# Performance work log

Hardware: AMD Instinct MI355X
Metric: run time of the kernel (lower is better)

## Reference

```python
import jax, jax.numpy as jnp
import numpy as np

# NLMConv1DBlock: NLM LogicMachine(depth=2, breadth=2, input_dims=[0, inp_dim, 3],
# output_dims=[D,D,D], logic_hidden_dim=None -> each logic MLP is Linear+Sigmoid),
# followed by swish -> Conv1d(D, D, k=3, pad=1) over the t axis -> swish.
# Only the unary (arity-1) output of the second NLM layer is consumed, so the
# nullary/binary heads of layer 2 are never computed (their params are unused).


def swish(x):
    return x * jax.nn.sigmoid(x)


def lin_sig(x, W, b):
    # LogicInference with logic_hidden_dim=None: single Linear + Sigmoid
    return jax.nn.sigmoid(x @ W.T + b)


def reduce_unary(f1):
    # Reducer(dim=1): [B, n, C] -> [B, 2C]; exclude_self is a no-op for arity 1.
    # Channels interleaved as (exists_0, forall_0, exists_1, forall_1, ...)
    e = jnp.max(f1, axis=1)
    a = jnp.min(f1, axis=1)
    return jnp.stack([e, a], axis=-1).reshape(f1.shape[0], -1)


def reduce_pair(f2):
    # Reducer(dim=2, exclude_self=True): [B, n, n, C] -> [B, n, 2C].
    # Diagonal (i==j) masked to 0 for exists(max) and 1 for forall(min);
    # reduction over the second object index (axis=2). Interleaved exists/forall.
    n = f2.shape[1]
    eye = jnp.eye(n, dtype=bool)[None, :, :, None]
    e = jnp.max(jnp.where(eye, jnp.zeros((), f2.dtype), f2), axis=2)
    a = jnp.min(jnp.where(eye, jnp.ones((), f2.dtype), f2), axis=2)
    return jnp.stack([e, a], axis=-1).reshape(f2.shape[0], n, -1)


def perm2(f2):
    # Permutation(dim=2): concat identity and object-dim transpose along channels
    return jnp.concatenate([f2, jnp.swapaxes(f2, 1, 2)], axis=-1)


def setup_inputs() -> dict:
    key = jax.random.key(0)
    ks = jax.random.split(key, 12)
    b, t, n, inp_dim, D = 16, 16, 64, 2, 32
    s = 0.1
    x = jax.random.normal(ks[0], (b, t, n, inp_dim), jnp.float32)
    # Layer 1 logic MLPs (forward concat order: [expand, input, reduce])
    W1_0 = jax.random.normal(ks[1], (D, 2 * inp_dim), jnp.float32) * s        # nullary: reduce(unary) -> 2*inp_dim
    b1_0 = jax.random.normal(ks[2], (D,), jnp.float32) * s
    W1_1 = jax.random.normal(ks[3], (D, inp_dim + 6), jnp.float32) * s        # unary: [x, reduce(cmp)] -> inp_dim + 2*3
    b1_1 = jax.random.normal(ks[4], (D,), jnp.float32) * s
    W1_2 = jax.random.normal(ks[5], (D, 2 * (inp_dim + 3)), jnp.float32) * s  # binary: perm2([expand(x), cmp])
    b1_2 = jax.random.normal(ks[6], (D,), jnp.float32) * s
    # Layer 2, only the unary head is used downstream
    W2_1 = jax.random.normal(ks[7], (D, 4 * D), jnp.float32) * s              # [expand(g0), g1, reduce(g2)]
    b2_1 = jax.random.normal(ks[8], (D,), jnp.float32) * s
    # Conv1d(D, D, kernel_size=3, padding=1), OIH layout
    Wc = jax.random.normal(ks[9], (D, D, 3), jnp.float32) * s
    bc = jax.random.normal(ks[10], (D,), jnp.float32) * s
    return {"x": x, "W1_0": W1_0, "b1_0": b1_0, "W1_1": W1_1, "b1_1": b1_1,
            "W1_2": W1_2, "b1_2": b1_2, "W2_1": W2_1, "b2_1": b2_1,
            "Wc": Wc, "bc": bc}


def reference(x, W1_0, b1_0, W1_1, b1_1, W1_2, b1_2, W2_1, b2_1, Wc, bc):
    b, t, n, c = x.shape
    B = b * t
    xf = x.reshape(B, n, c)

    # pairwise relational inputs: [B, n, n, 3]
    ar = jnp.arange(n)
    base = jnp.stack([ar[:, None] < ar[None, :], ar[:, None] == ar[None, :]],
                     axis=-1).astype(x.dtype)                       # [n, n, 2], batch-invariant
    numbers = xf[:, :, 1]
    cmp3 = (numbers[:, :, None] < numbers[:, None, :]).astype(x.dtype)
    cmp = jnp.concatenate([jnp.broadcast_to(base[None], (B, n, n, 2)),
                           cmp3[..., None]], axis=-1)

    # --- NLM layer 1 (input dims [0, c, 3]) ---
    g0 = lin_sig(reduce_unary(xf), W1_0, b1_0)                                # [B, D]
    g1 = lin_sig(jnp.concatenate([xf, reduce_pair(cmp)], axis=-1), W1_1, b1_1)  # [B, n, D]
    f2 = jnp.concatenate([jnp.broadcast_to(xf[:, :, None, :], (B, n, n, c)), cmp], axis=-1)
    g2 = lin_sig(perm2(f2), W1_2, b1_2)                                       # [B, n, n, D]

    # --- NLM layer 2, unary head only (block takes nlm(...)[1]) ---
    D = g1.shape[-1]
    h1_in = jnp.concatenate([jnp.broadcast_to(g0[:, None, :], (B, n, D)),
                             g1, reduce_pair(g2)], axis=-1)                   # [B, n, 4D]
    h1 = swish(lin_sig(h1_in, W2_1, b2_1))                                    # [B, n, D]

    # (b t) n c -> (b n) c t, conv1d over t, -> b t n c, swish
    y = h1.reshape(b, t, n, D).transpose(0, 2, 3, 1).reshape(b * n, D, t)
    y = jax.lax.conv_general_dilated(y, Wc, (1,), [(1, 1)],
                                     dimension_numbers=('NCH', 'OIH', 'NCH'))
    y = y + bc[None, :, None]
    y = y.reshape(b, n, D, t).transpose(0, 3, 1, 2)
    return swish(y)
```

## Files before the change

### kernel.cpp

```cpp
#include <hip/hip_runtime.h>

#define NN 64
#define DD 32

__device__ __forceinline__ float sigmoidf_(float x) {
    return 1.0f / (1.0f + __expf(-x));
}

__device__ __forceinline__ float rlanef_(float v, int l) {
    return __int_as_float(__builtin_amdgcn_readlane(__float_as_int(v), l));
}

__global__ __launch_bounds__(1024) void stage1_kernel(
    const float* __restrict__ x,
    const float* __restrict__ W1_0, const float* __restrict__ b1_0,
    const float* __restrict__ W1_1, const float* __restrict__ b1_1,
    const float* __restrict__ W1_2, const float* __restrict__ b1_2,
    const float* __restrict__ W2_1, const float* __restrict__ b2_1,
    float* __restrict__ h1ws)
{
    __shared__ __align__(16) float sx0[NN];
    __shared__ __align__(16) float sx1[NN];
    __shared__ __align__(16) float sFeat[NN][100];
    __shared__ __align__(16) float sW2p[DD][100];
    __shared__ float sW12[DD*10];
    __shared__ float sB12[DD];
    __shared__ float sW11t[8*DD];
    __shared__ float sB11[DD];
    __shared__ float sG0[DD];
    __shared__ float sZ0[DD];
    __shared__ float sEC2[NN];
    __shared__ float sAC2[NN];

    const int tid = threadIdx.x;
    const int bb  = blockIdx.x;
    const int d   = tid & 31;

    if (tid < NN) {
        sx0[tid] = x[(bb*NN + tid)*2 + 0];
        sx1[tid] = x[(bb*NN + tid)*2 + 1];
    }
    for (int idx = tid; idx < DD*96; idx += 1024) {
        int dr = idx / 96, kp = idx - dr*96;
        sW2p[dr][kp] = W2_1[dr*128 + 32 + kp];
    }
    if (tid < 320) {
        sW12[tid] = W1_2[tid];
    } else if (tid < 352) {
        sB12[tid - 320] = b1_2[tid - 320];
    } else if (tid < 608) {
        int idx = tid - 352; int dr = idx >> 3, c = idx & 7;
        sW11t[c*DD + dr] = W1_1[idx];
    } else if (tid < 640) {
        sB11[tid - 608] = b1_1[tid - 608];
    }
    __syncthreads();

    const float myx0 = sx0[tid & 63];
    const float myx1 = sx1[tid & 63];

    const float w0 = sW12[d*10+0], w1 = sW12[d*10+1], w2 = sW12[d*10+2],
                w4 = sW12[d*10+4], w5 = sW12[d*10+5], w6 = sW12[d*10+6],
                w7 = sW12[d*10+7], w9 = sW12[d*10+9];
    const float bw = sB12[d];

    if (tid < NN) {
        float ni = sx1[tid];
        float mx = -1e30f, mn = 1e30f;
        for (int j = 0; j < NN; ++j) {
            float nj = sx1[j];
            bool v = (j != tid);
            mx = fmaxf(mx, v ? nj : -1e30f);
            mn = fminf(mn, v ? nj :  1e30f);
        }
        sEC2[tid] = (ni < mx) ? 1.0f : 0.0f;
        sAC2[tid] = (ni < mn) ? 1.0f : 0.0f;
    } else if (tid < 96) {
        int dd = tid - 64;
        float mx0 = -1e30f, mn0 = 1e30f, mx1 = -1e30f, mn1 = 1e30f;
        for (int j = 0; j < NN; ++j) {
            float a = sx0[j], c = sx1[j];
            mx0 = fmaxf(mx0, a); mn0 = fminf(mn0, a);
            mx1 = fmaxf(mx1, c); mn1 = fminf(mn1, c);
        }
        float z = mx0*W1_0[dd*4+0] + mn0*W1_0[dd*4+1]
                + mx1*W1_0[dd*4+2] + mn1*W1_0[dd*4+3] + b1_0[dd];
        sG0[dd] = sigmoidf_(z);
    }
    __syncthreads();

    if (tid < 32) {
        float z = b2_1[tid];
        const float* wr = W2_1 + tid*128;
        #pragma unroll
        for (int k = 0; k < 32; ++k) z += sG0[k]*wr[k];
        sZ0[tid] = z;
    }

    {
        const int ia = tid >> 5;
        const int ib = ia + 32;
        const float na = sx1[ia], nb = sx1[ib];
        const float Aa = sx0[ia]*w0 + na*w1 + bw;
        const float Ab = sx0[ib]*w0 + nb*w1 + bw;
        const float A24a = Aa + w2 + w4, A29a = Aa + w2 + w9;
        const float A74a = Aa + w7 + w4, A79a = Aa + w7 + w9;
        const float A24b = Ab + w2 + w4, A29b = Ab + w2 + w9;
        const float A74b = Ab + w7 + w4, A79b = Ab + w7 + w9;
        float smaxa = -1e30f, smina = 1e30f;
        float smaxb = -1e30f, sminb = 1e30f;

        #pragma unroll
        for (int j = 0; j < 32; ++j) {
            const float x0j = rlanef_(myx0, j);
            const float x1j = rlanef_(myx1, j);
            const float bv  = x0j*w5 + x1j*w6;
            const float tb = ((nb < x1j) ? A74b : A79b) + bv;
            smaxb = fmaxf(smaxb, tb);
            sminb = fminf(sminb, tb);
            const bool ca = (na < x1j);
            const float t2 = ca ? A24a : A29a;
            const float t7 = ca ? A74a : A79a;
            const float ta = ((ia < j) ? t2 : t7) + bv;
            const bool va = (j != ia);
            smaxa = fmaxf(smaxa, va ? ta : -1e30f);
            smina = fminf(smina, va ? ta :  1e30f);
        }
        #pragma unroll
        for (int j = 32; j < 64; ++j) {
            const float x0j = rlanef_(myx0, j);
            const float x1j = rlanef_(myx1, j);
            const float bv  = x0j*w5 + x1j*w6;
            const float ta = ((na < x1j) ? A24a : A29a) + bv;
            smaxa = fmaxf(smaxa, ta);
            smina = fminf(smina, ta);
            const bool cb = (nb < x1j);
            const float t2 = cb ? A24b : A29b;
            const float t7 = cb ? A74b : A79b;
            const float tb = ((ib < j) ? t2 : t7) + bv;
            const bool vb = (j != ib);
            smaxb = fmaxf(smaxb, vb ? tb : -1e30f);
            sminb = fminf(sminb, vb ? tb :  1e30f);
        }
        *(float2*)&sFeat[ia][32 + 2*d] = make_float2(sigmoidf_(smaxa), sigmoidf_(smina));
        *(float2*)&sFeat[ib][32 + 2*d] = make_float2(sigmoidf_(smaxb), sigmoidf_(sminb));

        float z1a = sx0[ia]*sW11t[0*DD+d] + na*sW11t[1*DD+d]
                  + sW11t[2*DD+d]
                  + ((ia == 0) ? sW11t[3*DD+d] : 0.0f)
                  + sEC2[ia]*sW11t[6*DD+d] + sAC2[ia]*sW11t[7*DD+d] + sB11[d];
        sFeat[ia][d] = sigmoidf_(z1a);
        float z1b = sx0[ib]*sW11t[0*DD+d] + nb*sW11t[1*DD+d]
                  + ((ib < NN-1) ? sW11t[2*DD+d] : 0.0f)
                  + sEC2[ib]*sW11t[6*DD+d] + sAC2[ib]*sW11t[7*DD+d] + sB11[d];
        sFeat[ib][d] = sigmoidf_(z1b);
    }
    __syncthreads();

    if (tid < 256) {
        const int i0 = tid >> 4;
        const int dh = tid & 15;
        const float* f0 = sFeat[i0];
        const float* f1 = sFeat[i0+16];
        const float* f2 = sFeat[i0+32];
        const float* f3 = sFeat[i0+48];
        const float* wA = sW2p[dh];
        const float* wB = sW2p[dh+16];
        const float z0A = sZ0[dh], z0B = sZ0[dh+16];
        float a0A = z0A, a0B = z0B, a1A = z0A, a1B = z0B;
        float a2A = z0A, a2B = z0B, a3A = z0A, a3B = z0B;
        #pragma unroll
        for (int kc = 0; kc < 96; kc += 4) {
            const float4 pa = *(const float4*)(wA + kc);
            const float4 pb = *(const float4*)(wB + kc);
            const float4 v0 = *(const float4*)(f0 + kc);
            const float4 v1 = *(const float4*)(f1 + kc);
            const float4 v2 = *(const float4*)(f2 + kc);
            const float4 v3 = *(const float4*)(f3 + kc);
            a0A += v0.x*pa.x + v0.y*pa.y + v0.z*pa.z + v0.w*pa.w;
            a0B += v0.x*pb.x + v0.y*pb.y + v0.z*pb.z + v0.w*pb.w;
            a1A += v1.x*pa.x + v1.y*pa.y + v1.z*pa.z + v1.w*pa.w;
            a1B += v1.x*pb.x + v1.y*pb.y + v1.z*pb.z + v1.w*pb.w;
            a2A += v2.x*pa.x + v2.y*pa.y + v2.z*pa.z + v2.w*pa.w;
            a2B += v2.x*pb.x + v2.y*pb.y + v2.z*pb.z + v2.w*pb.w;
            a3A += v3.x*pa.x + v3.y*pa.y + v3.z*pa.z + v3.w*pa.w;
            a3B += v3.x*pb.x + v3.y*pb.y + v3.z*pb.z + v3.w*pb.w;
        }
        float* orow = h1ws + bb*(NN*DD);
        float h;
        h = sigmoidf_(a0A); orow[ i0     *DD + dh]      = h * sigmoidf_(h);
        h = sigmoidf_(a0B); orow[ i0     *DD + dh + 16] = h * sigmoidf_(h);
        h = sigmoidf_(a1A); orow[(i0+16)*DD + dh]       = h * sigmoidf_(h);
        h = sigmoidf_(a1B); orow[(i0+16)*DD + dh + 16]  = h * sigmoidf_(h);
        h = sigmoidf_(a2A); orow[(i0+32)*DD + dh]       = h * sigmoidf_(h);
        h = sigmoidf_(a2B); orow[(i0+32)*DD + dh + 16]  = h * sigmoidf_(h);
        h = sigmoidf_(a3A); orow[(i0+48)*DD + dh]       = h * sigmoidf_(h);
        h = sigmoidf_(a3B); orow[(i0+48)*DD + dh + 16]  = h * sigmoidf_(h);
    }
}

__global__ __launch_bounds__(512) void conv_kernel(
    const float* __restrict__ h1ws,
    const float* __restrict__ Wc,
    const float* __restrict__ bc,
    float* __restrict__ out)
{
    __shared__ __align__(16) float sh[4][18][32];

    const int tid = threadIdx.x;
    const int blk = blockIdx.x;
    const int b   = blk >> 4;
    const int n0  = (blk & 15) * 4;
    const int t   = tid >> 5;
    const int dd  = tid & 31;

    float wreg[96];
    {
        const float* wrow = Wc + dd*96;
        #pragma unroll
        for (int c = 0; c < 24; ++c) {
            float4 v = *(const float4*)(wrow + c*4);
            wreg[c*4+0] = v.x; wreg[c*4+1] = v.y;
            wreg[c*4+2] = v.z; wreg[c*4+3] = v.w;
        }
    }
    for (int idx = tid; idx < 4*16*32; idx += 512) {
        int nl = idx >> 9; int rem = idx & 511;
        int tl = rem >> 5; int dl = rem & 31;
        sh[nl][tl+1][dl] = h1ws[((b*16 + tl)*NN + (n0+nl))*DD + dl];
    }
    if (tid < 256) {
        int nl = tid >> 6; int r = tid & 63;
        int row = (r >> 5) * 17; int dl = r & 31;
        sh[nl][row][dl] = 0.0f;
    }
    const float bcv = bc[dd];
    __syncthreads();

    #pragma unroll
    for (int g = 0; g < 4; ++g) {
        float acc = bcv;
        const float* r0 = &sh[g][t][0];
        const float* r1 = &sh[g][t+1][0];
        const float* r2 = &sh[g][t+2][0];
        #pragma unroll
        for (int c = 0; c < 8; ++c) {
            float4 f0  = *(const float4*)(r0 + c*4);
            float4 f1  = *(const float4*)(r1 + c*4);
            float4 f2v = *(const float4*)(r2 + c*4);
            const int q = c*12;
            acc += f0.x*wreg[q+0] + f1.x*wreg[q+1]  + f2v.x*wreg[q+2];
            acc += f0.y*wreg[q+3] + f1.y*wreg[q+4]  + f2v.y*wreg[q+5];
            acc += f0.z*wreg[q+6] + f1.z*wreg[q+7]  + f2v.z*wreg[q+8];
            acc += f0.w*wreg[q+9] + f1.w*wreg[q+10] + f2v.w*wreg[q+11];
        }
        out[((b*16 + t)*NN + (n0+g))*DD + dd] = acc * sigmoidf_(acc);
    }
}

extern "C" void kernel_launch(void* const* d_in, const int* in_sizes, int n_in,
                              void* d_out, int out_size, void* d_ws, size_t ws_size,
                              hipStream_t stream) {
    const float* x    = (const float*)d_in[0];
    const float* W1_0 = (const float*)d_in[1];
    const float* b1_0 = (const float*)d_in[2];
    const float* W1_1 = (const float*)d_in[3];
    const float* b1_1 = (const float*)d_in[4];
    const float* W1_2 = (const float*)d_in[5];
    const float* b1_2 = (const float*)d_in[6];
    const float* W2_1 = (const float*)d_in[7];
    const float* b2_1 = (const float*)d_in[8];
    const float* Wc   = (const float*)d_in[9];
    const float* bc   = (const float*)d_in[10];

    float* h1buf = (float*)d_out;
    float* out   = (float*)d_out;

    stage1_kernel<<<256, 1024, 0, stream>>>(x, W1_0, b1_0, W1_1, b1_1,
                                            W1_2, b1_2, W2_1, b2_1, h1buf);
    conv_kernel<<<256, 512, 0, stream>>>(h1buf, Wc, bc, out);
}
```

Baseline: 97.56 us.

## Fuse NLM stage and temporal conv into one kernel with per-node-group blocks

Each block now handles one batch and one group of 4 objects across all 16 timesteps, rather than one (b,t) slice, so the conv over t can run from shared memory inside the same kernel. This removes the h1 round trip through global memory and the second launch. Wave shuffle reductions replace the serial min/max loops, and closed-form comparisons replace the exists/forall tables for cmp. In exchange, each block redoes the nullary and reduction work for every t, and register pressure at 1024 threads per block goes up.

```diff
diff --git a/kernel.cpp b/kernel.cpp
--- a/kernel.cpp
+++ b/kernel.cpp
@@ -11,98 +11,92 @@
     return __int_as_float(__builtin_amdgcn_readlane(__float_as_int(v), l));
 }
 
-__global__ __launch_bounds__(1024) void stage1_kernel(
+__global__ __launch_bounds__(1024) void fused_kernel(
     const float* __restrict__ x,
     const float* __restrict__ W1_0, const float* __restrict__ b1_0,
     const float* __restrict__ W1_1, const float* __restrict__ b1_1,
     const float* __restrict__ W1_2, const float* __restrict__ b1_2,
     const float* __restrict__ W2_1, const float* __restrict__ b2_1,
-    float* __restrict__ h1ws)
+    const float* __restrict__ Wc,   const float* __restrict__ bc,
+    float* __restrict__ out)
 {
-    __shared__ __align__(16) float sx0[NN];
-    __shared__ __align__(16) float sx1[NN];
-    __shared__ __align__(16) float sFeat[NN][100];
-    __shared__ __align__(16) float sW2p[DD][100];
-    __shared__ float sW12[DD*10];
-    __shared__ float sB12[DD];
-    __shared__ float sW11t[8*DD];
-    __shared__ float sB11[DD];
-    __shared__ float sG0[DD];
-    __shared__ float sZ0[DD];
-    __shared__ float sEC2[NN];
-    __shared__ float sAC2[NN];
+    __shared__ __align__(16) float sx0[16][64];
+    __shared__ __align__(16) float sx1[16][64];
+    __shared__ __align__(16) float sFeat[64][100];
+    __shared__ __align__(16) float sW2p[32][100];
+    __shared__ __align__(16) float sW2a[32][33];
+    __shared__ __align__(16) float sH1[18][4][32];
+    __shared__ float sW12[320], sB12[32];
+    __shared__ float sW11t[256], sB11[32];
+    __shared__ float sW10[128], sB10[32], sB21[32];
+    __shared__ float sZ0[16][32];
 
     const int tid = threadIdx.x;
-    const int bb  = blockIdx.x;
-    const int d   = tid & 31;
-
-    if (tid < NN) {
-        sx0[tid] = x[(bb*NN + tid)*2 + 0];
-        sx1[tid] = x[(bb*NN + tid)*2 + 1];
-    }
-    for (int idx = tid; idx < DD*96; idx += 1024) {
+    const int bq  = blockIdx.x;
+    const int b   = bq >> 4;
+    const int qn  = bq & 15;
+
+    {
+        int t = tid >> 6, j = tid & 63;
+        float2 v = *(const float2*)&x[((b*16 + t)*64 + j)*2];
+        sx0[t][j] = v.x; sx1[t][j] = v.y;
+    }
+    for (int idx = tid; idx < 32*96; idx += 1024) {
         int dr = idx / 96, kp = idx - dr*96;
         sW2p[dr][kp] = W2_1[dr*128 + 32 + kp];
     }
-    if (tid < 320) {
-        sW12[tid] = W1_2[tid];
-    } else if (tid < 352) {
-        sB12[tid - 320] = b1_2[tid - 320];
-    } else if (tid < 608) {
-        int idx = tid - 352; int dr = idx >> 3, c = idx & 7;
-        sW11t[c*DD + dr] = W1_1[idx];
-    } else if (tid < 640) {
-        sB11[tid - 608] = b1_1[tid - 608];
-    }
+    {
+        int dr = tid >> 5, k = tid & 31;
+        sW2a[dr][k] = W2_1[dr*128 + k];
+    }
+    if (tid < 320) sW12[tid] = W1_2[tid];
+    else if (tid < 352) sB12[tid-320] = b1_2[tid-320];
+    else if (tid < 608) { int i2 = tid-352; sW11t[(i2&7)*32 + (i2>>3)] = W1_1[i2]; }
+    else if (tid < 640) sB11[tid-608] = b1_1[tid-608];
+    else if (tid < 768) sW10[tid-640] = W1_0[tid-640];
+    else if (tid < 800) sB10[tid-768] = b1_0[tid-768];
+    else if (tid < 832) sB21[tid-800] = b2_1[tid-800];
+    if (tid < 128) { int m = (tid>>5)&3, dl = tid&31; sH1[0][m][dl] = 0.0f; sH1[17][m][dl] = 0.0f; }
     __syncthreads();
 
-    const float myx0 = sx0[tid & 63];
-    const float myx1 = sx1[tid & 63];
-
-    const float w0 = sW12[d*10+0], w1 = sW12[d*10+1], w2 = sW12[d*10+2],
-                w4 = sW12[d*10+4], w5 = sW12[d*10+5], w6 = sW12[d*10+6],
-                w7 = sW12[d*10+7], w9 = sW12[d*10+9];
-    const float bw = sB12[d];
-
-    if (tid < NN) {
-        float ni = sx1[tid];
-        float mx = -1e30f, mn = 1e30f;
-        for (int j = 0; j < NN; ++j) {
-            float nj = sx1[j];
-            bool v = (j != tid);
-            mx = fmaxf(mx, v ? nj : -1e30f);
-            mn = fminf(mn, v ? nj :  1e30f);
-        }
-        sEC2[tid] = (ni < mx) ? 1.0f : 0.0f;
-        sAC2[tid] = (ni < mn) ? 1.0f : 0.0f;
-    } else if (tid < 96) {
-        int dd = tid - 64;
-        float mx0 = -1e30f, mn0 = 1e30f, mx1 = -1e30f, mn1 = 1e30f;
-        for (int j = 0; j < NN; ++j) {
-            float a = sx0[j], c = sx1[j];
-            mx0 = fmaxf(mx0, a); mn0 = fminf(mn0, a);
-            mx1 = fmaxf(mx1, c); mn1 = fminf(mn1, c);
-        }
-        float z = mx0*W1_0[dd*4+0] + mn0*W1_0[dd*4+1]
-                + mx1*W1_0[dd*4+2] + mn1*W1_0[dd*4+3] + b1_0[dd];
-        sG0[dd] = sigmoidf_(z);
-    }
-    __syncthreads();
-
-    if (tid < 32) {
-        float z = b2_1[tid];
-        const float* wr = W2_1 + tid*128;
-        #pragma unroll
-        for (int k = 0; k < 32; ++k) z += sG0[k]*wr[k];
-        sZ0[tid] = z;
-    }
-
-    {
-        const int ia = tid >> 5;
+    {
+        const int t    = tid >> 6;
+        const int lane = tid & 63;
+        const int mm   = lane >> 5;
+        const int d    = lane & 31;
+
+        const float myx0 = sx0[t][lane];
+        const float myx1 = sx1[t][lane];
+
+        float mx0 = myx0, mn0 = myx0, mx1 = myx1, mn1 = myx1;
+        #pragma unroll
+        for (int off = 1; off < 64; off <<= 1) {
+            mx0 = fmaxf(mx0, __shfl_xor(mx0, off));
+            mn0 = fminf(mn0, __shfl_xor(mn0, off));
+            mx1 = fmaxf(mx1, __shfl_xor(mx1, off));
+            mn1 = fminf(mn1, __shfl_xor(mn1, off));
+        }
+        const float g0reg = sigmoidf_(mx0*sW10[d*4+0] + mn0*sW10[d*4+1]
+                                    + mx1*sW10[d*4+2] + mn1*sW10[d*4+3] + sB10[d]);
+        {
+            float z = sB21[d];
+            #pragma unroll
+            for (int k = 0; k < 32; ++k)
+                z += rlanef_(g0reg, k) * sW2a[d][k];
+            if (mm == 0) sZ0[t][d] = z;
+        }
+
+        const float w0 = sW12[d*10+0], w1 = sW12[d*10+1], w2 = sW12[d*10+2],
+                    w4 = sW12[d*10+4], w5 = sW12[d*10+5], w6 = sW12[d*10+6],
+                    w7 = sW12[d*10+7], w9 = sW12[d*10+9];
+        const float bw = sB12[d];
+
+        const int ia = qn + (mm << 4);
         const int ib = ia + 32;
-        const float na = sx1[ia], nb = sx1[ib];
-        const float Aa = sx0[ia]*w0 + na*w1 + bw;
-        const float Ab = sx0[ib]*w0 + nb*w1 + bw;
+        const float na  = sx1[t][ia], xa0 = sx0[t][ia];
+        const float nb  = sx1[t][ib], xb0 = sx0[t][ib];
+        const float Aa = xa0*w0 + na*w1 + bw;
+        const float Ab = xb0*w0 + nb*w1 + bw;
         const float A24a = Aa + w2 + w4, A29a = Aa + w2 + w9;
         const float A74a = Aa + w7 + w4, A79a = Aa + w7 + w9;
         const float A24b = Ab + w2 + w4, A29b = Ab + w2 + w9;
@@ -142,119 +136,120 @@
             smaxb = fmaxf(smaxb, vb ? tb : -1e30f);
             sminb = fminf(sminb, vb ? tb :  1e30f);
         }
-        *(float2*)&sFeat[ia][32 + 2*d] = make_float2(sigmoidf_(smaxa), sigmoidf_(smina));
-        *(float2*)&sFeat[ib][32 + 2*d] = make_float2(sigmoidf_(smaxb), sigmoidf_(sminb));
-
-        float z1a = sx0[ia]*sW11t[0*DD+d] + na*sW11t[1*DD+d]
-                  + sW11t[2*DD+d]
-                  + ((ia == 0) ? sW11t[3*DD+d] : 0.0f)
-                  + sEC2[ia]*sW11t[6*DD+d] + sAC2[ia]*sW11t[7*DD+d] + sB11[d];
-        sFeat[ia][d] = sigmoidf_(z1a);
-        float z1b = sx0[ib]*sW11t[0*DD+d] + nb*sW11t[1*DD+d]
-                  + ((ib < NN-1) ? sW11t[2*DD+d] : 0.0f)
-                  + sEC2[ib]*sW11t[6*DD+d] + sAC2[ib]*sW11t[7*DD+d] + sB11[d];
-        sFeat[ib][d] = sigmoidf_(z1b);
+        const int ra = t*4 + mm;
+        const int rb = ra + 2;
+        *(float2*)&sFeat[ra][32 + 2*d] = make_float2(sigmoidf_(smaxa), sigmoidf_(smina));
+        *(float2*)&sFeat[rb][32 + 2*d] = make_float2(sigmoidf_(smaxb), sigmoidf_(sminb));
+
+        float z1a = xa0*sW11t[0*32+d] + na*sW11t[1*32+d]
+                  + sW11t[2*32+d]
+                  + ((ia == 0)   ? sW11t[3*32+d] : 0.0f)
+                  + ((na < mx1)  ? sW11t[6*32+d] : 0.0f)
+                  + ((na == mn1) ? sW11t[7*32+d] : 0.0f) + sB11[d];
+        sFeat[ra][d] = sigmoidf_(z1a);
+        float z1b = xb0*sW11t[0*32+d] + nb*sW11t[1*32+d]
+                  + ((ib < 63)   ? sW11t[2*32+d] : 0.0f)
+                  + ((nb < mx1)  ? sW11t[6*32+d] : 0.0f)
+                  + ((nb == mn1) ? sW11t[7*32+d] : 0.0f) + sB11[d];
+        sFeat[rb][d] = sigmoidf_(z1b);
     }
     __syncthreads();
 
-    if (tid < 256) {
-        const int i0 = tid >> 4;
+    const int dc = tid & 31;
+    const float* wrow = Wc + dc*96;
+    float4 wv0[12];
+    #pragma unroll
+    for (int c = 0; c < 12; ++c) wv0[c] = *(const float4*)(wrow + c*4);
+    const float bcv = bc[dc];
+
+    if (tid < 512) {
+        const int rp = tid >> 4;
         const int dh = tid & 15;
-        const float* f0 = sFeat[i0];
-        const float* f1 = sFeat[i0+16];
-        const float* f2 = sFeat[i0+32];
-        const float* f3 = sFeat[i0+48];
+        const float* fA = sFeat[rp];
+        const float* fB = sFeat[rp+32];
         const float* wA = sW2p[dh];
         const float* wB = sW2p[dh+16];
-        const float z0A = sZ0[dh], z0B = sZ0[dh+16];
-        float a0A = z0A, a0B = z0B, a1A = z0A, a1B = z0B;
-        float a2A = z0A, a2B = z0B, a3A = z0A, a3B = z0B;
+        float a00 = sZ0[rp>>2][dh],     a01 = sZ0[rp>>2][dh+16];
+        float a10 = sZ0[(rp>>2)+8][dh], a11 = sZ0[(rp>>2)+8][dh+16];
         #pragma unroll
         for (int kc = 0; kc < 96; kc += 4) {
             const float4 pa = *(const float4*)(wA + kc);
             const float4 pb = *(const float4*)(wB + kc);
-            const float4 v0 = *(const float4*)(f0 + kc);
-            const float4 v1 = *(const float4*)(f1 + kc);
-            const float4 v2 = *(const float4*)(f2 + kc);
-            const float4 v3 = *(const float4*)(f3 + kc);
-            a0A += v0.x*pa.x + v0.y*pa.y + v0.z*pa.z + v0.w*pa.w;
-            a0B += v0.x*pb.x + v0.y*pb.y + v0.z*pb.z + v0.w*pb.w;
-            a1A += v1.x*pa.x + v1.y*pa.y + v1.z*pa.z + v1.w*pa.w;
-            a1B += v1.x*pb.x + v1.y*pb.y + v1.z*pb.z + v1.w*pb.w;
-            a2A += v2.x*pa.x + v2.y*pa.y + v2.z*pa.z + v2.w*pa.w;
-            a2B += v2.x*pb.x + v2.y*pb.y + v2.z*pb.z + v2.w*pb.w;
-            a3A += v3.x*pa.x + v3.y*pa.y + v3.z*pa.z + v3.w*pa.w;
-            a3B += v3.x*pb.x + v3.y*pb.y + v3.z*pb.z + v3.w*pb.w;
-        }
-        float* orow = h1ws + bb*(NN*DD);
+            const float4 va = *(const float4*)(fA + kc);
+            const float4 vb = *(const float4*)(fB + kc);
+            a00 += va.x*pa.x + va.y*pa.y + va.z*pa.z + va.w*pa.w;
+            a01 += va.x*pb.x + va.y*pb.y + va.z*pb.z + va.w*pb.w;
+            a10 += vb.x*pa.x + vb.y*pa.y + vb.z*pa.z + vb.w*pa.w;
+            a11 += vb.x*pb.x + vb.y*pb.y + vb.z*pb.z + vb.w*pb.w;
+        }
         float h;
-        h = sigmoidf_(a0A); orow[ i0     *DD + dh]      = h * sigmoidf_(h);
-        h = sigmoidf_(a0B); orow[ i0     *DD + dh + 16] = h * sigmoidf_(h);
-        h = sigmoidf_(a1A); orow[(i0+16)*DD + dh]       = h * sigmoidf_(h);
-        h = sigmoidf_(a1B); orow[(i0+16)*DD + dh + 16]  = h * sigmoidf_(h);
-        h = sigmoidf_(a2A); orow[(i0+32)*DD + dh]       = h * sigmoidf_(h);
-        h = sigmoidf_(a2B); orow[(i0+32)*DD + dh + 16]  = h * sigmoidf_(h);
-        h = sigmoidf_(a3A); orow[(i0+48)*DD + dh]       = h * sigmoidf_(h);
-        h = sigmoidf_(a3B); orow[(i0+48)*DD + dh + 16]  = h * sigmoidf_(h);
-    }
-}
-
-__global__ __launch_bounds__(512) void conv_kernel(
-    const float* __restrict__ h1ws,
-    const float* __restrict__ Wc,
-    const float* __restrict__ bc,
-    float* __restrict__ out)
-{
-    __shared__ __align__(16) float sh[4][18][32];
-
-    const int tid = threadIdx.x;
-    const int blk = blockIdx.x;
-    const int b   = blk >> 4;
-    const int n0  = (blk & 15) * 4;
-    const int t   = tid >> 5;
-    const int dd  = tid & 31;
-
-    float wreg[96];
-    {
-        const float* wrow = Wc + dd*96;
-        #pragma unroll
-        for (int c = 0; c < 24; ++c) {
-            float4 v = *(const float4*)(wrow + c*4);
-            wreg[c*4+0] = v.x; wreg[c*4+1] = v.y;
-            wreg[c*4+2] = v.z; wreg[c*4+3] = v.w;
-        }
-    }
-    for (int idx = tid; idx < 4*16*32; idx += 512) {
-        int nl = idx >> 9; int rem = idx & 511;
-        int tl = rem >> 5; int dl = rem & 31;
-        sh[nl][tl+1][dl] = h1ws[((b*16 + tl)*NN + (n0+nl))*DD + dl];
-    }
-    if (tid < 256) {
-        int nl = tid >> 6; int r = tid & 63;
-        int row = (r >> 5) * 17; int dl = r & 31;
-        sh[nl][row][dl] = 0.0f;
-    }
-    const float bcv = bc[dd];
+        h = sigmoidf_(a00); sH1[(rp>>2)+1][rp&3][dh]    = h * sigmoidf_(h);
+        h = sigmoidf_(a01); sH1[(rp>>2)+1][rp&3][dh+16] = h * sigmoidf_(h);
+        h = sigmoidf_(a10); sH1[(rp>>2)+9][rp&3][dh]    = h * sigmoidf_(h);
+        h = sigmoidf_(a11); sH1[(rp>>2)+9][rp&3][dh+16] = h * sigmoidf_(h);
+    }
     __syncthreads();
 
-    #pragma unroll
-    for (int g = 0; g < 4; ++g) {
-        float acc = bcv;
-        const float* r0 = &sh[g][t][0];
-        const float* r1 = &sh[g][t+1][0];
-        const float* r2 = &sh[g][t+2][0];
-        #pragma unroll
-        for (int c = 0; c < 8; ++c) {
-            float4 f0  = *(const float4*)(r0 + c*4);
-            float4 f1  = *(const float4*)(r1 + c*4);
-            float4 f2v = *(const float4*)(r2 + c*4);
-            const int q = c*12;
-            acc += f0.x*wreg[q+0] + f1.x*wreg[q+1]  + f2v.x*wreg[q+2];
-            acc += f0.y*wreg[q+3] + f1.y*wreg[q+4]  + f2v.y*wreg[q+5];
-            acc += f0.z*wreg[q+6] + f1.z*wreg[q+7]  + f2v.z*wreg[q+8];
-            acc += f0.w*wreg[q+9] + f1.w*wreg[q+10] + f2v.w*wreg[q+11];
-        }
-        out[((b*16 + t)*NN + (n0+g))*DD + dd] = acc * sigmoidf_(acc);
+    {
+        const int gg = tid >> 9;
+        const int tt = (tid >> 5) & 15;
+        const int gQ = gg + 2;
+
+        float wk[48];
+        #pragma unroll
+        for (int c = 0; c < 12; ++c) {
+            wk[c*4+0] = wv0[c].x; wk[c*4+1] = wv0[c].y;
+            wk[c*4+2] = wv0[c].z; wk[c*4+3] = wv0[c].w;
+        }
+        float4 wv1[12];
+        #pragma unroll
+        for (int c = 0; c < 12; ++c) wv1[c] = *(const float4*)(wrow + 48 + c*4);
+
+        float accP = bcv, accQ = bcv;
+        #pragma unroll
+        for (int c = 0; c < 4; ++c) {
+            const int qk = c*12;
+            float4 f0 = *(const float4*)&sH1[tt  ][gg][c*4];
+            float4 f1 = *(const float4*)&sH1[tt+1][gg][c*4];
+            float4 f2 = *(const float4*)&sH1[tt+2][gg][c*4];
+            accP += f0.x*wk[qk+0] + f1.x*wk[qk+1]  + f2.x*wk[qk+2];
+            accP += f0.y*wk[qk+3] + f1.y*wk[qk+4]  + f2.y*wk[qk+5];
+            accP += f0.z*wk[qk+6] + f1.z*wk[qk+7]  + f2.z*wk[qk+8];
+            accP += f0.w*wk[qk+9] + f1.w*wk[qk+10] + f2.w*wk[qk+11];
+            f0 = *(const float4*)&sH1[tt  ][gQ][c*4];
+            f1 = *(const float4*)&sH1[tt+1][gQ][c*4];
+            f2 = *(const float4*)&sH1[tt+2][gQ][c*4];
+            accQ += f0.x*wk[qk+0] + f1.x*wk[qk+1]  + f2.x*wk[qk+2];
+            accQ += f0.y*wk[qk+3] + f1.y*wk[qk+4]  + f2.y*wk[qk+5];
+            accQ += f0.z*wk[qk+6] + f1.z*wk[qk+7]  + f2.z*wk[qk+8];
+            accQ += f0.w*wk[qk+9] + f1.w*wk[qk+10] + f2.w*wk[qk+11];
+        }
+        float wkB[48];
+        #pragma unroll
+        for (int c = 0; c < 12; ++c) {
+            wkB[c*4+0] = wv1[c].x; wkB[c*4+1] = wv1[c].y;
+            wkB[c*4+2] = wv1[c].z; wkB[c*4+3] = wv1[c].w;
+        }
+        #pragma unroll
+        for (int c = 4; c < 8; ++c) {
+            const int qk = (c-4)*12;
+            float4 f0 = *(const float4*)&sH1[tt  ][gg][c*4];
+            float4 f1 = *(const float4*)&sH1[tt+1][gg][c*4];
+            float4 f2 = *(const float4*)&sH1[tt+2][gg][c*4];
+            accP += f0.x*wkB[qk+0] + f1.x*wkB[qk+1]  + f2.x*wkB[qk+2];
+            accP += f0.y*wkB[qk+3] + f1.y*wkB[qk+4]  + f2.y*wkB[qk+5];
+            accP += f0.z*wkB[qk+6] + f1.z*wkB[qk+7]  + f2.z*wkB[qk+8];
+            accP += f0.w*wkB[qk+9] + f1.w*wkB[qk+10] + f2.w*wkB[qk+11];
+            f0 = *(const float4*)&sH1[tt  ][gQ][c*4];
+            f1 = *(const float4*)&sH1[tt+1][gQ][c*4];
+            f2 = *(const float4*)&sH1[tt+2][gQ][c*4];
+            accQ += f0.x*wkB[qk+0] + f1.x*wkB[qk+1]  + f2.x*wkB[qk+2];
+            accQ += f0.y*wkB[qk+3] + f1.y*wkB[qk+4]  + f2.y*wkB[qk+5];
+            accQ += f0.z*wkB[qk+6] + f1.z*wkB[qk+7]  + f2.z*wkB[qk+8];
+            accQ += f0.w*wkB[qk+9] + f1.w*wkB[qk+10] + f2.w*wkB[qk+11];
+        }
+        out[((b*16 + tt)*64 + (qn + 16*gg))*32 + dc] = accP * sigmoidf_(accP);
+        out[((b*16 + tt)*64 + (qn + 16*gQ))*32 + dc] = accQ * sigmoidf_(accQ);
     }
 }
 
@@ -273,10 +268,7 @@
     const float* Wc   = (const float*)d_in[9];
     const float* bc   = (const float*)d_in[10];
 
-    float* h1buf = (float*)d_out;
-    float* out   = (float*)d_out;
-
-    stage1_kernel<<<256, 1024, 0, stream>>>(x, W1_0, b1_0, W1_1, b1_1,
-                                            W1_2, b1_2, W2_1, b2_1, h1buf);
-    conv_kernel<<<256, 512, 0, stream>>>(h1buf, Wc, bc, out);
-}
+    fused_kernel<<<256, 1024, 0, stream>>>(x, W1_0, b1_0, W1_1, b1_1,
+                                           W1_2, b1_2, W2_1, b2_1,
+                                           Wc, bc, (float*)d_out);
+}
```

Measured after the change: 98.19 us. Within noise of the previous version (+0.6%).
